# Performance work log

Measured on AMD Instinct MI355X. Metric: run time of the kernel, lower is better.

Reference implementation:

```python
import jax, jax.numpy as jnp
import numpy as np
import math

EMBED_DIM = 1024
NUM_HEADS = 16
HEAD_DIM = EMBED_DIM // NUM_HEADS
B, T = 2, 2048


def setup_inputs() -> dict:
    key = jax.random.key(0)
    ks = jax.random.split(key, 8)
    x = jax.random.normal(ks[0], (B, T, EMBED_DIM), dtype=jnp.float32)
    context_vector = jax.random.normal(ks[1], (B, T, EMBED_DIM), dtype=jnp.float32)
    # causal mask: 1 where attention allowed, 0 elsewhere (mask==0 -> -1e9)
    mask = jnp.tril(jnp.ones((T, T), dtype=jnp.int32))[None, None, :, :]
    # Xavier-uniform projections (fan_in = fan_out = EMBED_DIM)
    limit = math.sqrt(6.0 / (EMBED_DIM + EMBED_DIM))
    def xavier(k):
        return jax.random.uniform(k, (EMBED_DIM, EMBED_DIM), jnp.float32, -limit, limit)
    w_q = xavier(ks[2])
    w_k = xavier(ks[3])
    w_v = xavier(ks[4])
    w_o = xavier(ks[5])
    b_o = jnp.zeros((EMBED_DIM,), jnp.float32)
    context_bias = jnp.zeros((EMBED_DIM,), jnp.float32)
    return {"x": x, "mask": mask, "context_vector": context_vector,
            "w_q": w_q, "w_k": w_k, "w_v": w_v, "w_o": w_o, "b_o": b_o,
            "context_bias": context_bias}


def reference(x, mask, context_vector, w_q, w_k, w_v, w_o, b_o, context_bias):
    Bx, Tx, C = x.shape
    H, hd = NUM_HEADS, HEAD_DIM
    # nn.Linear: y = x @ W^T
    q = x @ w_q.T + context_bias * context_vector  # [B,T,C]
    k = x @ w_k.T
    v = x @ w_v.T
    q = q.reshape(Bx, Tx, H, hd).transpose(0, 2, 1, 3)  # [B,H,T,hd]
    k = k.reshape(Bx, Tx, H, hd).transpose(0, 2, 1, 3)
    v = v.reshape(Bx, Tx, H, hd).transpose(0, 2, 1, 3)
    scores = jnp.einsum('bhqd,bhkd->bhqk', q, k) / math.sqrt(hd)  # [B,H,T,T]
    scores = jnp.where(mask == 0, jnp.float32(-1e9), scores)
    attn = jax.nn.softmax(scores, axis=-1)  # dropout p=0 (eval) -> identity
    out = jnp.einsum('bhqk,bhkd->bhqd', attn, v)  # [B,H,T,hd]
    out = out.transpose(0, 2, 1, 3).reshape(Bx, Tx, C)
    return out @ w_o.T + b_o
```

## Files before the change

kernel.cpp:

```cpp
#include <hip/hip_runtime.h>

typedef __bf16 bf16_t;
typedef __attribute__((ext_vector_type(8))) __bf16 bf16x8;
typedef __attribute__((ext_vector_type(4))) __bf16 bf16x4;
typedef __attribute__((ext_vector_type(2))) __bf16 bf16x2;
typedef __attribute__((ext_vector_type(4))) float floatx4;
typedef __attribute__((ext_vector_type(4))) unsigned uintx4;

#define LOG2E 1.4426950408889634f

__device__ __forceinline__ void async16(const void* g, void* l) {
  __builtin_amdgcn_global_load_lds(
      (const __attribute__((address_space(1))) void*)g,
      (__attribute__((address_space(3))) void*)l, 16, 0, 0);
}

__global__ __launch_bounds__(256) void cast_all(
    const float* __restrict__ x, const float* __restrict__ wq,
    const float* __restrict__ wk, const float* __restrict__ wv,
    const float* __restrict__ wo, bf16_t* __restrict__ dst) {
  int i = (blockIdx.x * 256 + threadIdx.x) * 4;
  const float* src;
  int off;
  if (i < 4194304) {
    src = x; off = i;
  } else {
    int j = i - 4194304;
    int w = j >> 20;
    off = j & 1048575;
    src = (w == 0) ? wq : (w == 1) ? wk : (w == 2) ? wv : wo;
  }
  float4 v = *(const float4*)(src + off);
  bf16x4 o;
  o[0] = (bf16_t)v.x; o[1] = (bf16_t)v.y; o[2] = (bf16_t)v.z; o[3] = (bf16_t)v.w;
  *(bf16x4*)(dst + i) = o;
}

__device__ __forceinline__ void gemm128(const bf16_t* __restrict__ A,
                                        const bf16_t* __restrict__ W,
                                        int tileM, int tileN, char* smem,
                                        floatx4 acc[4][4]) {
  bf16_t* As = (bf16_t*)smem;
  bf16_t* Bs = (bf16_t*)(smem + 16384);
  const int tid = threadIdx.x;
  const int lane = tid & 63;
  const int quad = lane >> 4;
  const int l15 = lane & 15;
  const int wid = tid >> 6;
  const int waveM = (wid >> 1) << 6;
  const int waveN = (wid & 1) << 6;
  const int swz = l15 & 7;
  for (int i = 0; i < 4; ++i)
    for (int j = 0; j < 4; ++j)
      for (int r = 0; r < 4; ++r) acc[i][j][r] = 0.0f;

  const int r0 = tid >> 3;
  const int sc = ((tid & 7) ^ (r0 & 7)) << 3;
  const size_t abase = (size_t)(tileM + r0) * 1024 + sc;
  const size_t bbase = (size_t)(tileN + r0) * 1024 + sc;
  const int ldbase = (tid & ~63) * 16;

  for (int kt = 0; kt < 1024; kt += 64) {
    if (kt) __syncthreads();
    for (int j = 0; j < 4; ++j) {
      async16(A + abase + (size_t)j * 32 * 1024 + kt, smem + j * 4096 + ldbase);
      async16(W + bbase + (size_t)j * 32 * 1024 + kt, smem + 16384 + j * 4096 + ldbase);
    }
    __syncthreads();
    for (int kk = 0; kk < 2; ++kk) {
      const int cq = (((kk << 2) + quad) ^ swz) << 3;
      bf16x8 af[4], bfr[4];
      for (int rb = 0; rb < 4; ++rb)
        af[rb] = *(const bf16x8*)&As[(waveM + rb * 16 + l15) * 64 + cq];
      for (int cb = 0; cb < 4; ++cb)
        bfr[cb] = *(const bf16x8*)&Bs[(waveN + cb * 16 + l15) * 64 + cq];
      for (int rb = 0; rb < 4; ++rb)
        for (int cb = 0; cb < 4; ++cb)
          acc[rb][cb] = __builtin_amdgcn_mfma_f32_16x16x32_bf16(af[rb], bfr[cb],
                                                                acc[rb][cb], 0, 0, 0);
    }
  }
}

__device__ __forceinline__ void gemm64x128(const bf16_t* __restrict__ A,
                                           const bf16_t* __restrict__ W,
                                           int tileM, int tileN, char* smem,
                                           floatx4 acc[2][4]) {
  bf16_t* As = (bf16_t*)smem;
  bf16_t* Bs = (bf16_t*)(smem + 8192);
  const int tid = threadIdx.x;
  const int lane = tid & 63;
  const int quad = lane >> 4;
  const int l15 = lane & 15;
  const int wid = tid >> 6;
  const int waveM = (wid >> 1) * 32;
  const int waveN = (wid & 1) * 64;
  const int swz = l15 & 7;
  for (int i = 0; i < 2; ++i)
    for (int j = 0; j < 4; ++j)
      for (int r = 0; r < 4; ++r) acc[i][j][r] = 0.0f;

  const int r0 = tid >> 3;
  const int sc = ((tid & 7) ^ (r0 & 7)) << 3;
  const size_t abase = (size_t)(tileM + r0) * 1024 + sc;
  const size_t bbase = (size_t)(tileN + r0) * 1024 + sc;
  const int ldbase = (tid & ~63) * 16;

  for (int kt = 0; kt < 1024; kt += 64) {
    if (kt) __syncthreads();
    for (int j = 0; j < 2; ++j)
      async16(A + abase + (size_t)j * 32 * 1024 + kt, smem + j * 4096 + ldbase);
    for (int j = 0; j < 4; ++j)
      async16(W + bbase + (size_t)j * 32 * 1024 + kt, smem + 8192 + j * 4096 + ldbase);
    __syncthreads();
    for (int kk = 0; kk < 2; ++kk) {
      const int cq = (((kk << 2) + quad) ^ swz) << 3;
      bf16x8 af[2], bfr[4];
      for (int rb = 0; rb < 2; ++rb)
        af[rb] = *(const bf16x8*)&As[(waveM + rb * 16 + l15) * 64 + cq];
      for (int cb = 0; cb < 4; ++cb)
        bfr[cb] = *(const bf16x8*)&Bs[(waveN + cb * 16 + l15) * 64 + cq];
      for (int rb = 0; rb < 2; ++rb)
        for (int cb = 0; cb < 4; ++cb)
          acc[rb][cb] = __builtin_amdgcn_mfma_f32_16x16x32_bf16(af[rb], bfr[cb],
                                                                acc[rb][cb], 0, 0, 0);
    }
  }
}

__global__ __launch_bounds__(256) void proj_qkv(
    const bf16_t* __restrict__ xb, const bf16_t* __restrict__ wq,
    const bf16_t* __restrict__ wk, const bf16_t* __restrict__ wv,
    const float* __restrict__ cbias, const float* __restrict__ cv,
    bf16_t* __restrict__ qb, bf16_t* __restrict__ kb, bf16_t* __restrict__ vtb) {
  __shared__ __align__(16) char smem[128 * 136 * 2];
  const int mode = blockIdx.z;
  const bf16_t* W = (mode == 0) ? wq : ((mode == 1) ? wk : wv);
  const int tileM = blockIdx.y * 128, tileN = blockIdx.x * 128;
  floatx4 acc[4][4];
  gemm128(xb, W, tileM, tileN, smem, acc);
  const int tid = threadIdx.x, lane = tid & 63, quad = lane >> 4, l15 = lane & 15,
            wid = tid >> 6;
  const int waveM = (wid >> 1) << 6, waveN = (wid & 1) << 6;
  bf16_t* T = (bf16_t*)smem;
  __syncthreads();
  for (int rb = 0; rb < 4; ++rb)
    for (int cb = 0; cb < 4; ++cb)
      for (int r = 0; r < 4; ++r) {
        int rl = waveM + rb * 16 + quad * 4 + r;
        int cl = waveN + cb * 16 + l15;
        float v = acc[rb][cb][r];
        if (mode == 0)
          v += cbias[tileN + cl] * cv[(size_t)(tileM + rl) * 1024 + tileN + cl];
        if (mode == 2)
          T[cl * 136 + rl] = (bf16_t)v;
        else
          T[rl * 136 + cl] = (bf16_t)v;
      }
  __syncthreads();
  const int rowi = tid >> 1, half = tid & 1;
  const bf16_t* src = T + rowi * 136 + half * 64;
  if (mode == 2) {
    int n = tileN + rowi;
    int b = tileM >> 11;
    int t0 = (tileM & 2047) + half * 64;
    bf16_t* dst = vtb + ((size_t)b * 1024 + n) * 2048 + t0;
    for (int i = 0; i < 8; ++i) *(bf16x8*)(dst + i * 8) = *(const bf16x8*)(src + i * 8);
  } else {
    int tg = tileM + rowi;
    int b = tg >> 11, t = tg & 2047;
    int n0 = tileN + half * 64;
    int h = n0 >> 6;
    bf16_t* base = (mode == 0) ? qb : kb;
    bf16_t* dst = base + ((size_t)(b * 16 + h) * 2048 + t) * 64;
    for (int i = 0; i < 8; ++i) *(bf16x8*)(dst + i * 8) = *(const bf16x8*)(src + i * 8);
  }
}

__global__ __launch_bounds__(256) void attn_fwd(
    const bf16_t* __restrict__ qb, const bf16_t* __restrict__ kb,
    const bf16_t* __restrict__ vtb, bf16_t* __restrict__ ob) {
  __shared__ __align__(16) bf16_t Qs[64 * 64];
  __shared__ __align__(16) bf16_t Ks[2][64 * 64];
  __shared__ __align__(16) bf16_t Vs[2][64 * 64];
  const int bh = blockIdx.x;
  const int qt = 31 - blockIdx.y;
  const int q0 = qt * 64;
  const int tid = threadIdx.x, lane = tid & 63, w = tid >> 6, quad = lane >> 4,
            l15 = lane & 15;

  const int sr = tid >> 3;
  const int sc = (tid & 7) ^ (sr & 7);
  const int ldst = (tid & ~63) * 16;
  const int swz = l15 & 7;

  {
    const bf16_t* gq = qb + ((size_t)bh * 2048 + q0 + sr) * 64 + sc * 8;
    async16(gq, (char*)Qs + ldst);
    async16(gq + 32 * 64, (char*)Qs + ldst + 4096);
  }

  floatx4 O[4];
  for (int d = 0; d < 4; ++d)
    for (int r = 0; r < 4; ++r) O[d][r] = 0.f;
  float m_c = -1e30f, l_c = 0.f;
  const float SC = 0.125f * LOG2E;

  {
    const bf16_t* gk = kb + ((size_t)bh * 2048 + sr) * 64 + sc * 8;
    async16(gk, (char*)Ks[0] + ldst);
    async16(gk + 32 * 64, (char*)Ks[0] + ldst + 4096);
    const bf16_t* gv = vtb + ((size_t)bh * 64 + sr) * 2048 + sc * 8;
    async16(gv, (char*)Vs[0] + ldst);
    async16(gv + (size_t)32 * 2048, (char*)Vs[0] + ldst + 4096);
  }
  __syncthreads();

  bf16x8 qf[2];
  for (int ks = 0; ks < 2; ++ks) {
    const int cq = (ks * 4 + quad) ^ swz;
    qf[ks] = *(const bf16x8*)&Qs[(w * 16 + l15) * 64 + cq * 8];
  }

  for (int kt = 0; kt <= qt; ++kt) {
    const int cur = kt & 1;
    if (kt < qt) {
      const int nxt = cur ^ 1;
      const bf16_t* gk2 = kb + ((size_t)bh * 2048 + (kt + 1) * 64 + sr) * 64 + sc * 8;
      async16(gk2, (char*)Ks[nxt] + ldst);
      async16(gk2 + 32 * 64, (char*)Ks[nxt] + ldst + 4096);
      const bf16_t* gv2 = vtb + ((size_t)bh * 64 + sr) * 2048 + (size_t)(kt + 1) * 64 + sc * 8;
      async16(gv2, (char*)Vs[nxt] + ldst);
      async16(gv2 + (size_t)32 * 2048, (char*)Vs[nxt] + ldst + 4096);
    }
    floatx4 s[4];
    for (int i = 0; i < 4; ++i)
      for (int r = 0; r < 4; ++r) s[i][r] = 0.f;
    for (int ks = 0; ks < 2; ++ks) {
      const int cq = (ks * 4 + quad) ^ swz;
      for (int kbt = 0; kbt < 4; ++kbt) {
        bf16x8 kf = *(const bf16x8*)&Ks[cur][(kbt * 16 + l15) * 64 + cq * 8];
        s[kbt] = __builtin_amdgcn_mfma_f32_16x16x32_bf16(kf, qf[ks], s[kbt], 0, 0, 0);
      }
    }
    if (kt == qt) {
      const int qloc = w * 16 + l15;
      for (int kbt = 0; kbt < 4; ++kbt)
        for (int r = 0; r < 4; ++r)
          if (kbt * 16 + quad * 4 + r > qloc) s[kbt][r] = -1e30f;
    }
    float mx = s[0][0];
    for (int i = 0; i < 4; ++i)
      for (int r = 0; r < 4; ++r) mx = fmaxf(mx, s[i][r]);
    mx = fmaxf(mx, __shfl_xor(mx, 16));
    mx = fmaxf(mx, __shfl_xor(mx, 32));
    const float m_new = fmaxf(m_c, mx);
    const float alpha = exp2f((m_c - m_new) * SC);
    const float msc = m_new * SC;
    m_c = m_new;
    float p[4][4];
    float rs = 0.f;
    for (int i = 0; i < 4; ++i)
      for (int r = 0; r < 4; ++r) {
        float v = exp2f(fmaf(s[i][r], SC, -msc));
        p[i][r] = v;
        rs += v;
      }
    rs += __shfl_xor(rs, 16);
    rs += __shfl_xor(rs, 32);
    l_c = l_c * alpha + rs;
    for (int db = 0; db < 4; ++db)
      for (int r = 0; r < 4; ++r) O[db][r] *= alpha;
    unsigned pk[4][2];
    for (int i = 0; i < 4; ++i)
      for (int rr = 0; rr < 2; ++rr) {
        bf16x2 t2;
        t2[0] = (bf16_t)p[i][2 * rr];
        t2[1] = (bf16_t)p[i][2 * rr + 1];
        pk[i][rr] = __builtin_bit_cast(unsigned, t2);
      }
    for (int c = 0; c < 2; ++c) {
      uintx4 bw;
      bw[0] = pk[2 * c][0];
      bw[1] = pk[2 * c][1];
      bw[2] = pk[2 * c + 1][0];
      bw[3] = pk[2 * c + 1][1];
      bf16x8 pfrag = __builtin_bit_cast(bf16x8, bw);
      const int ch0 = (4 * c + (quad >> 1)) ^ swz;
      const int ch1 = (4 * c + 2 + (quad >> 1)) ^ swz;
      const int sub = (quad & 1) * 4;
      for (int db = 0; db < 4; ++db) {
        const bf16_t* vrow = &Vs[cur][(db * 16 + l15) * 64];
        bf16x4 lo = *(const bf16x4*)(vrow + ch0 * 8 + sub);
        bf16x4 hi = *(const bf16x4*)(vrow + ch1 * 8 + sub);
        bf16x8 vf;
        for (int e = 0; e < 4; ++e) { vf[e] = lo[e]; vf[e + 4] = hi[e]; }
        O[db] = __builtin_amdgcn_mfma_f32_16x16x32_bf16(vf, pfrag, O[db], 0, 0, 0);
      }
    }
    __syncthreads();
  }
  const int b = bh >> 4, h = bh & 15;
  const float inv = 1.0f / l_c;
  const int t = q0 + w * 16 + l15;
  for (int db = 0; db < 4; ++db) {
    bf16x4 o4;
    for (int r = 0; r < 4; ++r) o4[r] = (bf16_t)(O[db][r] * inv);
    *(bf16x4*)&ob[((size_t)b * 2048 + t) * 1024 + h * 64 + db * 16 + quad * 4] = o4;
  }
}

__global__ __launch_bounds__(256) void proj_o(
    const bf16_t* __restrict__ ain, const bf16_t* __restrict__ wo,
    const float* __restrict__ bo, float* __restrict__ out) {
  __shared__ __align__(16) char smem[24576];
  const int tileM = blockIdx.y * 64, tileN = blockIdx.x * 128;
  floatx4 acc[2][4];
  gemm64x128(ain, wo, tileM, tileN, smem, acc);
  const int tid = threadIdx.x, lane = tid & 63, quad = lane >> 4, l15 = lane & 15,
            wid = tid >> 6;
  const int waveM = (wid >> 1) * 32, waveN = (wid & 1) * 64;
  for (int rb = 0; rb < 2; ++rb)
    for (int cb = 0; cb < 4; ++cb)
      for (int r = 0; r < 4; ++r) {
        int row = tileM + waveM + rb * 16 + quad * 4 + r;
        int col = tileN + waveN + cb * 16 + l15;
        out[(size_t)row * 1024 + col] = acc[rb][cb][r] + bo[col];
      }
}

extern "C" void kernel_launch(void* const* d_in, const int* in_sizes, int n_in,
                              void* d_out, int out_size, void* d_ws, size_t ws_size,
                              hipStream_t stream) {
  const float* x     = (const float*)d_in[0];
  const float* cv    = (const float*)d_in[2];
  const float* wq    = (const float*)d_in[3];
  const float* wk    = (const float*)d_in[4];
  const float* wv    = (const float*)d_in[5];
  const float* wo    = (const float*)d_in[6];
  const float* bo    = (const float*)d_in[7];
  const float* cbias = (const float*)d_in[8];
  float* out = (float*)d_out;

  char* ws = (char*)d_ws;
  const size_t MB = 1 << 20;
  bf16_t* xb  = (bf16_t*)(ws + 0 * MB);
  bf16_t* wqb = (bf16_t*)(ws + 8 * MB);
  bf16_t* wkb = (bf16_t*)(ws + 10 * MB);
  bf16_t* wvb = (bf16_t*)(ws + 12 * MB);
  bf16_t* wob = (bf16_t*)(ws + 14 * MB);
  bf16_t* qb  = (bf16_t*)(ws + 16 * MB);
  bf16_t* kb  = (bf16_t*)(ws + 24 * MB);
  bf16_t* vtb = (bf16_t*)(ws + 32 * MB);
  bf16_t* ob  = (bf16_t*)(ws + 40 * MB);

  cast_all<<<8192, 256, 0, stream>>>(x, wq, wk, wv, wo, xb);
  proj_qkv<<<dim3(8, 32, 3), 256, 0, stream>>>(xb, wqb, wkb, wvb, cbias, cv, qb, kb, vtb);
  attn_fwd<<<dim3(32, 32), 256, 0, stream>>>(qb, kb, vtb, ob);
  proj_o<<<dim3(8, 64), 256, 0, stream>>>(ob, wob, bo, out);
}
```

Before: 224.0 us.

## Double-buffer GEMM k-tiles with async LDS prefetch and narrower k-step

Both projection GEMM helpers now split K into 32-wide tiles and keep two LDS buffers, so the next tile's async global-to-LDS load is issued before the MFMAs on the current tile run. This overlaps memory latency with compute and removes one barrier per iteration. The XOR swizzle and the load thread mapping are changed to fit the 32-column layout. In exchange there are twice as many loop iterations with half the MFMA work each, and the async loads are still waited on by the barrier every step, so overlap depends on how the compiler places the wait counters.

```diff
diff --git a/kernel.cpp b/kernel.cpp
--- a/kernel.cpp
+++ b/kernel.cpp
@@ -40,8 +40,6 @@
                                         const bf16_t* __restrict__ W,
                                         int tileM, int tileN, char* smem,
                                         floatx4 acc[4][4]) {
-  bf16_t* As = (bf16_t*)smem;
-  bf16_t* Bs = (bf16_t*)(smem + 16384);
   const int tid = threadIdx.x;
   const int lane = tid & 63;
   const int quad = lane >> 4;
@@ -49,36 +47,47 @@
   const int wid = tid >> 6;
   const int waveM = (wid >> 1) << 6;
   const int waveN = (wid & 1) << 6;
-  const int swz = l15 & 7;
+  const int swz = (l15 >> 1) & 3;
   for (int i = 0; i < 4; ++i)
     for (int j = 0; j < 4; ++j)
       for (int r = 0; r < 4; ++r) acc[i][j][r] = 0.0f;
 
-  const int r0 = tid >> 3;
-  const int sc = ((tid & 7) ^ (r0 & 7)) << 3;
+  const int r0 = tid >> 2;
+  const int sc = ((tid & 3) ^ ((r0 >> 1) & 3)) << 3;
   const size_t abase = (size_t)(tileM + r0) * 1024 + sc;
   const size_t bbase = (size_t)(tileN + r0) * 1024 + sc;
   const int ldbase = (tid & ~63) * 16;
 
-  for (int kt = 0; kt < 1024; kt += 64) {
-    if (kt) __syncthreads();
-    for (int j = 0; j < 4; ++j) {
-      async16(A + abase + (size_t)j * 32 * 1024 + kt, smem + j * 4096 + ldbase);
-      async16(W + bbase + (size_t)j * 32 * 1024 + kt, smem + 16384 + j * 4096 + ldbase);
-    }
+  async16(A + abase, smem + ldbase);
+  async16(A + abase + (size_t)64 * 1024, smem + 4096 + ldbase);
+  async16(W + bbase, smem + 8192 + ldbase);
+  async16(W + bbase + (size_t)64 * 1024, smem + 12288 + ldbase);
+  __syncthreads();
+
+  for (int kt = 0; kt < 32; ++kt) {
+    const int cur = kt & 1;
+    char* cb = smem + cur * 16384;
+    if (kt < 31) {
+      char* nb = smem + (cur ^ 1) * 16384;
+      const size_t ko = (size_t)(kt + 1) * 32;
+      async16(A + abase + ko, nb + ldbase);
+      async16(A + abase + (size_t)64 * 1024 + ko, nb + 4096 + ldbase);
+      async16(W + bbase + ko, nb + 8192 + ldbase);
+      async16(W + bbase + (size_t)64 * 1024 + ko, nb + 12288 + ldbase);
+    }
+    bf16_t* As = (bf16_t*)cb;
+    bf16_t* Bs = (bf16_t*)(cb + 8192);
+    const int cq = (quad ^ swz) << 3;
+    bf16x8 af[4], bfr[4];
+    for (int rb = 0; rb < 4; ++rb)
+      af[rb] = *(const bf16x8*)&As[(waveM + rb * 16 + l15) * 32 + cq];
+    for (int cbi = 0; cbi < 4; ++cbi)
+      bfr[cbi] = *(const bf16x8*)&Bs[(waveN + cbi * 16 + l15) * 32 + cq];
+    for (int rb = 0; rb < 4; ++rb)
+      for (int cbi = 0; cbi < 4; ++cbi)
+        acc[rb][cbi] = __builtin_amdgcn_mfma_f32_16x16x32_bf16(af[rb], bfr[cbi],
+                                                               acc[rb][cbi], 0, 0, 0);
     __syncthreads();
-    for (int kk = 0; kk < 2; ++kk) {
-      const int cq = (((kk << 2) + quad) ^ swz) << 3;
-      bf16x8 af[4], bfr[4];
-      for (int rb = 0; rb < 4; ++rb)
-        af[rb] = *(const bf16x8*)&As[(waveM + rb * 16 + l15) * 64 + cq];
-      for (int cb = 0; cb < 4; ++cb)
-        bfr[cb] = *(const bf16x8*)&Bs[(waveN + cb * 16 + l15) * 64 + cq];
-      for (int rb = 0; rb < 4; ++rb)
-        for (int cb = 0; cb < 4; ++cb)
-          acc[rb][cb] = __builtin_amdgcn_mfma_f32_16x16x32_bf16(af[rb], bfr[cb],
-                                                                acc[rb][cb], 0, 0, 0);
-    }
   }
 }
 
@@ -86,8 +95,6 @@
                                            const bf16_t* __restrict__ W,
                                            int tileM, int tileN, char* smem,
                                            floatx4 acc[2][4]) {
-  bf16_t* As = (bf16_t*)smem;
-  bf16_t* Bs = (bf16_t*)(smem + 8192);
   const int tid = threadIdx.x;
   const int lane = tid & 63;
   const int quad = lane >> 4;
@@ -95,36 +102,45 @@
   const int wid = tid >> 6;
   const int waveM = (wid >> 1) * 32;
   const int waveN = (wid & 1) * 64;
-  const int swz = l15 & 7;
+  const int swz = (l15 >> 1) & 3;
   for (int i = 0; i < 2; ++i)
     for (int j = 0; j < 4; ++j)
       for (int r = 0; r < 4; ++r) acc[i][j][r] = 0.0f;
 
-  const int r0 = tid >> 3;
-  const int sc = ((tid & 7) ^ (r0 & 7)) << 3;
+  const int r0 = tid >> 2;
+  const int sc = ((tid & 3) ^ ((r0 >> 1) & 3)) << 3;
   const size_t abase = (size_t)(tileM + r0) * 1024 + sc;
   const size_t bbase = (size_t)(tileN + r0) * 1024 + sc;
   const int ldbase = (tid & ~63) * 16;
 
-  for (int kt = 0; kt < 1024; kt += 64) {
-    if (kt) __syncthreads();
-    for (int j = 0; j < 2; ++j)
-      async16(A + abase + (size_t)j * 32 * 1024 + kt, smem + j * 4096 + ldbase);
-    for (int j = 0; j < 4; ++j)
-      async16(W + bbase + (size_t)j * 32 * 1024 + kt, smem + 8192 + j * 4096 + ldbase);
+  async16(A + abase, smem + ldbase);
+  async16(W + bbase, smem + 4096 + ldbase);
+  async16(W + bbase + (size_t)64 * 1024, smem + 8192 + ldbase);
+  __syncthreads();
+
+  for (int kt = 0; kt < 32; ++kt) {
+    const int cur = kt & 1;
+    char* cb = smem + cur * 12288;
+    if (kt < 31) {
+      char* nb = smem + (cur ^ 1) * 12288;
+      const size_t ko = (size_t)(kt + 1) * 32;
+      async16(A + abase + ko, nb + ldbase);
+      async16(W + bbase + ko, nb + 4096 + ldbase);
+      async16(W + bbase + (size_t)64 * 1024 + ko, nb + 8192 + ldbase);
+    }
+    bf16_t* As = (bf16_t*)cb;
+    bf16_t* Bs = (bf16_t*)(cb + 4096);
+    const int cq = (quad ^ swz) << 3;
+    bf16x8 af[2], bfr[4];
+    for (int rb = 0; rb < 2; ++rb)
+      af[rb] = *(const bf16x8*)&As[(waveM + rb * 16 + l15) * 32 + cq];
+    for (int cbi = 0; cbi < 4; ++cbi)
+      bfr[cbi] = *(const bf16x8*)&Bs[(waveN + cbi * 16 + l15) * 32 + cq];
+    for (int rb = 0; rb < 2; ++rb)
+      for (int cbi = 0; cbi < 4; ++cbi)
+        acc[rb][cbi] = __builtin_amdgcn_mfma_f32_16x16x32_bf16(af[rb], bfr[cbi],
+                                                               acc[rb][cbi], 0, 0, 0);
     __syncthreads();
-    for (int kk = 0; kk < 2; ++kk) {
-      const int cq = (((kk << 2) + quad) ^ swz) << 3;
-      bf16x8 af[2], bfr[4];
-      for (int rb = 0; rb < 2; ++rb)
-        af[rb] = *(const bf16x8*)&As[(waveM + rb * 16 + l15) * 64 + cq];
-      for (int cb = 0; cb < 4; ++cb)
-        bfr[cb] = *(const bf16x8*)&Bs[(waveN + cb * 16 + l15) * 64 + cq];
-      for (int rb = 0; rb < 2; ++rb)
-        for (int cb = 0; cb < 4; ++cb)
-          acc[rb][cb] = __builtin_amdgcn_mfma_f32_16x16x32_bf16(af[rb], bfr[cb],
-                                                                acc[rb][cb], 0, 0, 0);
-    }
   }
 }
 
```

After: 236.6 us. 1.06x slower.
